# Kernel optimization log

Hardware: AMD Instinct MI355X
Metric: run time of the kernel (lower is better)

Reference implementation:

```python
import jax, jax.numpy as jnp
import numpy as np

# Static graph layout: B equal-sized graphs so per-graph k is constant (jit-friendly).
NUM_GRAPHS = 128
NODES_PER_GRAPH = 1024
NUM_NODES = NUM_GRAPHS * NODES_PER_GRAPH  # 131072
NUM_EDGES = NUM_NODES * 32               # 4194304
CHANNELS = 256
RATIO = 0.5
K = max(1, int(NODES_PER_GRAPH * RATIO))  # 512, matches max(1, int(count*ratio))


def setup_inputs() -> dict:
    key = jax.random.key(0)
    k0, k1, k2, k3 = jax.random.split(key, 4)
    x = jax.random.normal(k0, (NUM_NODES, CHANNELS), dtype=jnp.float32)
    edge_index = jax.random.randint(k1, (2, NUM_EDGES), 0, NUM_NODES, dtype=jnp.int64)
    batch = (jnp.arange(NUM_NODES, dtype=jnp.int64) // NODES_PER_GRAPH)
    # score MLP params: Linear(C, C) -> tanh -> Linear(C, 1)
    s = 1.0 / np.sqrt(CHANNELS)
    W1 = jax.random.uniform(k2, (CHANNELS, CHANNELS), jnp.float32, -s, s)
    b1 = jnp.zeros((CHANNELS,), jnp.float32)
    W2 = jax.random.uniform(k3, (CHANNELS, 1), jnp.float32, -s, s)
    b2 = jnp.zeros((1,), jnp.float32)
    return {"x": x, "edge_index": edge_index, "batch": batch,
            "W1": W1, "b1": b1, "W2": W2, "b2": b2}


def reference(x, edge_index, batch, W1, b1, W2, b2):
    # Note: SAGPool.forward computes a GNN score then discards it and calls
    # super().forward, which recomputes scores with the self.score MLP. The GNN
    # path is dead code (and would error in torch); the effective math is below.
    scores = (jnp.tanh(x @ W1 + b1) @ W2 + b2)[:, 0]  # [num_nodes]

    # Per-graph top-k, vectorized across all graphs (equal-sized segments).
    s = scores.reshape(NUM_GRAPHS, NODES_PER_GRAPH)
    top_s, top_i = jax.lax.top_k(s, K)  # descending per graph, matches torch.topk
    offsets = (jnp.arange(NUM_GRAPHS, dtype=top_i.dtype) * NODES_PER_GRAPH)[:, None]
    perm = (top_i + offsets).reshape(-1)  # [B*K] global indices, graphs in order

    x_pooled = x[perm]
    batch_pooled = batch[perm]
    scores_pooled = top_s.reshape(-1)

    # Edge filtering: keep edges whose both endpoints survive.
    keep = jnp.zeros((NUM_NODES,), dtype=bool).at[perm].set(True)
    row, col = edge_index
    edge_mask = keep[row] & keep[col]
    # Static-shape compaction: stable-sort kept edges to the front, pad with -1.
    order = jnp.argsort(~edge_mask, stable=True)
    edge_index_pooled = jnp.where(edge_mask[order][None, :], edge_index[:, order], -1)

    return x_pooled, edge_index_pooled, batch_pooled, perm, scores_pooled
```

## Files before the change

### kernel.cpp

```cpp
#include <hip/hip_runtime.h>
#include <hip/hip_bf16.h>

#define NG 128
#define NPG 1024
#define NN (NG * NPG)
#define NE (NN * 32)
#define CH 256
#define KSEL 512

#define CAP 128
#define EPS 0.02f

#define OUT_X      0
#define OUT_EDGE   16777216
#define OUT_BATCH  25165824
#define OUT_PERM   25231360
#define OUT_SCORES 25296896

#define WS_SCORES  0
#define WS_KEEP    524288
#define WS_COUNTS  540672
#define WS_OFFSETS 544768
#define WS_BFRAG   548864
#define WS_BIDX    679936
#define WS_BSCORE  745472
#define WS_BN      811008
#define WS_BLO     811520

typedef __attribute__((ext_vector_type(8))) short bf16x8;
typedef __attribute__((ext_vector_type(4))) float f32x4;

__device__ __forceinline__ unsigned short f2bf(float f) {
    unsigned int b = __float_as_uint(f);
    return (unsigned short)((b + 0x7fffu + ((b >> 16) & 1u)) >> 16);
}

__device__ __forceinline__ float tanh_fast(float h) {
    const float e = __expf(2.0f * h);
    return 1.0f - 2.0f / (e + 1.0f);
}

__global__ __launch_bounds__(256)
void k_cvtW(const float* __restrict__ W1, unsigned short* __restrict__ W1b,
            unsigned int* __restrict__ keep_bits)
{
    const int t = blockIdx.x * 256 + threadIdx.x;
    if (t < NN / 32) keep_bits[t] = 0u;
    const int s    = t >> 10;
    const int rem  = t & 1023;
    const int n    = rem >> 6;
    const int lane = rem & 63;
    const int kbase = s * 32 + (lane >> 4) * 8;
    const int col   = n * 16 + (lane & 15);
    unsigned short u[8];
    #pragma unroll
    for (int j = 0; j < 8; ++j)
        u[j] = f2bf(W1[(size_t)(kbase + j) * CH + col]);
    uint4 v;
    v.x = u[0] | ((unsigned int)u[1] << 16);
    v.y = u[2] | ((unsigned int)u[3] << 16);
    v.z = u[4] | ((unsigned int)u[5] << 16);
    v.w = u[6] | ((unsigned int)u[7] << 16);
    *(uint4*)&W1b[(size_t)t * 8] = v;
}

__global__ __launch_bounds__(256, 3)
void k_mfma_scores(const float* __restrict__ x, const unsigned short* __restrict__ W1b,
                   const float* __restrict__ b1, const float* __restrict__ W2,
                   const float* __restrict__ b2, float* __restrict__ scores)
{
    __shared__ __align__(16) short As[64 * 256];
    __shared__ float epi[4][64];

    const int tid = threadIdx.x;
    const int w_  = tid >> 6;
    const int l   = tid & 63;
    const int n0  = blockIdx.x * 64;

    #pragma unroll
    for (int it = 0; it < 16; ++it) {
        const int flat = it * 1024 + tid * 4;
        const int row = flat >> 8;
        const int c   = flat & 255;
        const float4 v = *(const float4*)&x[(size_t)(n0 + row) * CH + c];
        uint2 p;
        p.x = f2bf(v.x) | ((unsigned int)f2bf(v.y) << 16);
        p.y = f2bf(v.z) | ((unsigned int)f2bf(v.w) << 16);
        const int byte = (row * 512 + c * 2) ^ ((row & 7) << 4);
        *(uint2*)((char*)As + byte) = p;
    }
    __syncthreads();

    f32x4 acc[4][4];
    #pragma unroll
    for (int m = 0; m < 4; ++m)
        #pragma unroll
        for (int n = 0; n < 4; ++n)
            acc[m][n] = (f32x4){0.f, 0.f, 0.f, 0.f};

    const unsigned short* Wl = W1b + l * 8;
    bf16x8 bc[4], bn[4];
    #pragma unroll
    for (int ni = 0; ni < 4; ++ni)
        bc[ni] = *(const bf16x8*)&Wl[(size_t)(w_ * 4 + ni) * 512];

    #pragma unroll
    for (int s = 0; s < 8; ++s) {
        if (s < 7) {
            #pragma unroll
            for (int ni = 0; ni < 4; ++ni)
                bn[ni] = *(const bf16x8*)&Wl[(size_t)((s + 1) * 16 + w_ * 4 + ni) * 512];
        }
        bf16x8 a[4];
        #pragma unroll
        for (int m = 0; m < 4; ++m) {
            const int row  = m * 16 + (l & 15);
            const int byte = (row * 512 + s * 64 + ((l >> 4) * 16)) ^ ((l & 7) << 4);
            a[m] = *(const bf16x8*)((const char*)As + byte);
        }
        #pragma unroll
        for (int ni = 0; ni < 4; ++ni)
            #pragma unroll
            for (int m = 0; m < 4; ++m)
                acc[m][ni] = __builtin_amdgcn_mfma_f32_16x16x32_bf16(a[m], bc[ni], acc[m][ni], 0, 0, 0);
        #pragma unroll
        for (int ni = 0; ni < 4; ++ni) bc[ni] = bn[ni];
    }

    float part[16];
    #pragma unroll
    for (int i = 0; i < 16; ++i) part[i] = 0.f;
    #pragma unroll
    for (int ni = 0; ni < 4; ++ni) {
        const int col = w_ * 64 + ni * 16 + (l & 15);
        const float b1c = b1[col];
        const float w2c = W2[col];
        #pragma unroll
        for (int m = 0; m < 4; ++m)
            #pragma unroll
            for (int r = 0; r < 4; ++r)
                part[m * 4 + r] += tanh_fast(acc[m][ni][r] + b1c) * w2c;
    }
    #pragma unroll
    for (int off = 1; off < 16; off <<= 1)
        #pragma unroll
        for (int i = 0; i < 16; ++i)
            part[i] += __shfl_xor(part[i], off, 64);

    if ((l & 15) == 0) {
        const int gq = l >> 4;
        #pragma unroll
        for (int m = 0; m < 4; ++m)
            #pragma unroll
            for (int r = 0; r < 4; ++r)
                epi[w_][m * 16 + gq * 4 + r] = part[m * 4 + r];
    }
    __syncthreads();
    if (tid < 64)
        scores[n0 + tid] = epi[0][tid] + epi[1][tid] + epi[2][tid] + epi[3][tid] + b2[0];
}

__global__ __launch_bounds__(256)
void k_topk(const float* __restrict__ scores, float* __restrict__ out,
            unsigned int* __restrict__ keep_bits, int* __restrict__ band_idx,
            int* __restrict__ band_n, int* __restrict__ band_lo)
{
    __shared__ float    sf[1024];
    __shared__ unsigned uk[1024];
    __shared__ int      hist[256];
    __shared__ int      cge[256];
    __shared__ unsigned s_prefix;
    __shared__ int      s_rank;
    __shared__ int      wtot[4];

    const int g = blockIdx.x;
    const int t = threadIdx.x;

    #pragma unroll
    for (int h = 0; h < 4; ++h) {
        const int i = h * 256 + t;
        const float f = scores[g * NPG + i];
        sf[i] = f;
        const unsigned b = __float_as_uint(f);
        uk[i] = (b & 0x80000000u) ? ~b : (b | 0x80000000u);
    }
    if (t == 0) { s_prefix = 0u; s_rank = KSEL; }
    __syncthreads();

    const unsigned pmaskv[4] = {0u, 0xFF000000u, 0xFFFF0000u, 0xFFFFFF00u};
    #pragma unroll
    for (int pass = 0; pass < 4; ++pass) {
        const int shift = 24 - pass * 8;
        hist[t] = 0;
        __syncthreads();
        const unsigned pm  = pmaskv[pass];
        const unsigned pfx = s_prefix;
        #pragma unroll
        for (int h = 0; h < 4; ++h) {
            const unsigned u = uk[h * 256 + t];
            if ((u & pm) == pfx) atomicAdd(&hist[(u >> shift) & 255], 1);
        }
        __syncthreads();
        cge[t] = hist[t];
        __syncthreads();
        #pragma unroll
        for (int off = 1; off < 256; off <<= 1) {
            const int v = (t + off < 256) ? cge[t + off] : 0;
            __syncthreads();
            cge[t] += v;
            __syncthreads();
        }
        const int r = s_rank;
        const int above = (t == 255) ? 0 : cge[t + 1];
        if (cge[t] >= r && above < r) {
            s_prefix = pfx | ((unsigned)t << shift);
            s_rank   = r - above;
        }
        __syncthreads();
    }

    const unsigned u512 = s_prefix;
    const unsigned fb = (u512 & 0x80000000u) ? (u512 & 0x7FFFFFFFu) : ~u512;
    const float tau = __uint_as_float(fb);

    bool cert[4], bnd[4];
    int myc = 0, myb = 0;
    #pragma unroll
    for (int j = 0; j < 4; ++j) {
        const float f = sf[t * 4 + j];
        cert[j] = (f > tau + EPS);
        bnd[j]  = (!cert[j]) && (f >= tau - EPS);
        myc += cert[j] ? 1 : 0;
        myb += bnd[j] ? 1 : 0;
    }
    const int pack = (myc << 16) | myb;
    const int lane = t & 63, w = t >> 6;
    int incl = pack;
    #pragma unroll
    for (int off = 1; off < 64; off <<= 1) {
        const int v = __shfl_up(incl, off, 64);
        if (lane >= off) incl += v;
    }
    if (lane == 63) wtot[w] = incl;
    __syncthreads();
    int wbase = 0;
    for (int i = 0; i < w; ++i) wbase += wtot[i];
    const int excl = wbase + incl - pack;
    int cpos = excl >> 16;
    int bpos = excl & 0xFFFF;
    const int total = wtot[0] + wtot[1] + wtot[2] + wtot[3];

    #pragma unroll
    for (int j = 0; j < 4; ++j) {
        const int li = t * 4 + j;
        if (cert[j]) {
            const int gi = g * NPG + li;
            out[OUT_PERM   + g * KSEL + cpos] = (float)gi;
            out[OUT_SCORES + g * KSEL + cpos] = sf[li];
            atomicOr(&keep_bits[gi >> 5], 1u << (gi & 31));
            ++cpos;
        } else if (bnd[j]) {
            if (bpos < CAP) band_idx[g * CAP + bpos] = li;
            ++bpos;
        }
    }
    out[OUT_BATCH + g * KSEL + t]       = (float)g;
    out[OUT_BATCH + g * KSEL + t + 256] = (float)g;
    if (t == 0) {
        band_lo[g] = (total >> 16);
        band_n[g]  = min(total & 0xFFFF, CAP);
    }
}

__global__ __launch_bounds__(256, 2)
void k_rescore(const float* __restrict__ x, const float* __restrict__ W1,
               const float* __restrict__ b1, const float* __restrict__ W2,
               const float* __restrict__ b2, const int* __restrict__ band_idx,
               const int* __restrict__ band_n, float* __restrict__ band_scores)
{
    const int g = blockIdx.x >> 2;
    const int c0 = (blockIdx.x & 3) * 32;
    if (band_n[g] <= c0) return;

    __shared__ __align__(16) float W1s[16][CH];
    __shared__ __align__(16) float Xs[32][16];

    const int tid = threadIdx.x;
    const int w_  = tid >> 6;
    const int l   = tid & 63;

    int iv = 0;
    if (w_ < 2) iv = band_idx[g * CAP + c0 + w_ * 16 + (l >> 2)] & 1023;
    const float* xg = x + ((size_t)g * NPG + iv) * CH;

    const float4 b1v = *(const float4*)&b1[l * 4];
    float acc[8][4];
    #pragma unroll
    for (int n = 0; n < 8; ++n) {
        acc[n][0] = b1v.x; acc[n][1] = b1v.y; acc[n][2] = b1v.z; acc[n][3] = b1v.w;
    }

    for (int kc = 0; kc < 16; ++kc) {
        __syncthreads();
        #pragma unroll
        for (int it = 0; it < 4; ++it) {
            const float* gp = W1 + (size_t)kc * (16 * CH) + (w_ * 4 + it) * CH + l * 4;
            float* lb = &W1s[0][0] + (w_ * 4 + it) * CH;
            __builtin_amdgcn_global_load_lds(
                (const __attribute__((address_space(1))) void*)gp,
                (__attribute__((address_space(3))) void*)lb, 16, 0, 0);
        }
        if (w_ < 2) {
            const float* gp = xg + kc * 16 + (l & 3) * 4;
            float* lb = &Xs[0][0] + w_ * 256;
            __builtin_amdgcn_global_load_lds(
                (const __attribute__((address_space(1))) void*)gp,
                (__attribute__((address_space(3))) void*)lb, 16, 0, 0);
        }
        __syncthreads();

        #pragma unroll
        for (int kq = 0; kq < 4; ++kq) {
            const int k4 = kq * 4;
            const float4 wv0 = *(const float4*)&W1s[k4 + 0][l * 4];
            const float4 wv1 = *(const float4*)&W1s[k4 + 1][l * 4];
            const float4 wv2 = *(const float4*)&W1s[k4 + 2][l * 4];
            const float4 wv3 = *(const float4*)&W1s[k4 + 3][l * 4];
            #pragma unroll
            for (int n = 0; n < 8; ++n) {
                const float4 xv = *(const float4*)&Xs[w_ * 8 + n][k4];
                acc[n][0] = fmaf(xv.x, wv0.x, acc[n][0]);
                acc[n][1] = fmaf(xv.x, wv0.y, acc[n][1]);
                acc[n][2] = fmaf(xv.x, wv0.z, acc[n][2]);
                acc[n][3] = fmaf(xv.x, wv0.w, acc[n][3]);
                acc[n][0] = fmaf(xv.y, wv1.x, acc[n][0]);
                acc[n][1] = fmaf(xv.y, wv1.y, acc[n][1]);
                acc[n][2] = fmaf(xv.y, wv1.z, acc[n][2]);
                acc[n][3] = fmaf(xv.y, wv1.w, acc[n][3]);
                acc[n][0] = fmaf(xv.z, wv2.x, acc[n][0]);
                acc[n][1] = fmaf(xv.z, wv2.y, acc[n][1]);
                acc[n][2] = fmaf(xv.z, wv2.z, acc[n][2]);
                acc[n][3] = fmaf(xv.z, wv2.w, acc[n][3]);
                acc[n][0] = fmaf(xv.w, wv3.x, acc[n][0]);
                acc[n][1] = fmaf(xv.w, wv3.y, acc[n][1]);
                acc[n][2] = fmaf(xv.w, wv3.z, acc[n][2]);
                acc[n][3] = fmaf(xv.w, wv3.w, acc[n][3]);
            }
        }
    }

    const float4 w2v = *(const float4*)&W2[l * 4];
    const float  bb  = b2[0];
    float s_[8];
    #pragma unroll
    for (int n = 0; n < 8; ++n) {
        s_[n] = tanhf(acc[n][0]) * w2v.x + tanhf(acc[n][1]) * w2v.y
              + tanhf(acc[n][2]) * w2v.z + tanhf(acc[n][3]) * w2v.w;
    }
    #pragma unroll
    for (int off = 1; off < 64; off <<= 1)
        #pragma unroll
        for (int n = 0; n < 8; ++n)
            s_[n] += __shfl_xor(s_[n], off, 64);

    if (l == 0) {
        #pragma unroll
        for (int n = 0; n < 8; ++n)
            band_scores[g * CAP + c0 + w_ * 8 + n] = s_[n] + bb;
    }
}

__global__ __launch_bounds__(64)
void k_bandsel(const float* __restrict__ band_scores, const int* __restrict__ band_idx,
               const int* __restrict__ band_n, const int* __restrict__ band_lo,
               float* __restrict__ out, unsigned int* __restrict__ keep_bits)
{
    __shared__ float bs[CAP];
    __shared__ int   bi[CAP];
    const int g = blockIdx.x;
    const int t = threadIdx.x;
    const int n  = band_n[g];
    const int lo = band_lo[g];
    int needed = KSEL - lo;
    if (needed > n) needed = n;

    #pragma unroll
    for (int h = 0; h < 2; ++h) {
        const int q = t + h * 64;
        const bool valid = q < n;
        bs[q] = valid ? band_scores[g * CAP + q] : -3.402823466e+38f;
        bi[q] = valid ? band_idx[g * CAP + q] : (NPG + q);
    }
    __syncthreads();
    for (int size = 2; size <= CAP; size <<= 1) {
        for (int stride = size >> 1; stride > 0; stride >>= 1) {
            __syncthreads();
            const int lo_i = ((t & ~(stride - 1)) << 1) | (t & (stride - 1));
            const int hi_i = lo_i + stride;
            const bool dirDesc = ((lo_i & size) == 0);
            const float va = bs[lo_i], vb = bs[hi_i];
            const int ia = bi[lo_i], ib = bi[hi_i];
            const bool aB = (va > vb) || (va == vb && ia < ib);
            if (aB != dirDesc) {
                bs[lo_i] = vb; bs[hi_i] = va;
                bi[lo_i] = ib; bi[hi_i] = ia;
            }
        }
    }
    __syncthreads();
    #pragma unroll
    for (int h = 0; h < 2; ++h) {
        const int s = t + h * 64;
        if (s < needed) {
            const int li = bi[s];
            const int gi = g * NPG + li;
            out[OUT_PERM   + g * KSEL + lo + s] = (float)gi;
            out[OUT_SCORES + g * KSEL + lo + s] = bs[s];
            atomicOr(&keep_bits[gi >> 5], 1u << (gi & 31));
        }
    }
}

__global__ __launch_bounds__(256)
void k_gather(const float* __restrict__ x, const float* __restrict__ perm_f,
              float* __restrict__ out_x)
{
    const int row  = blockIdx.x * 4 + (threadIdx.x >> 6);
    const int lane = threadIdx.x & 63;
    const int pi = (int)perm_f[row];
    const float4* src = (const float4*)&x[(size_t)pi * CH];
    float4* dst = (float4*)&out_x[(size_t)row * CH];
    dst[lane] = src[lane];
}

__global__ __launch_bounds__(256)
void k_edgecount(const int* __restrict__ ei, const unsigned int* __restrict__ keep_bits,
                 int* __restrict__ counts, float* __restrict__ out_edge)
{
    const int t = threadIdx.x;
    const float4 neg = make_float4(-1.f, -1.f, -1.f, -1.f);
    #pragma unroll
    for (int q = 0; q < 4; ++q) {
        ((float4*)out_edge)[(size_t)blockIdx.x * 1024 + q * 256 + t] = neg;
        ((float4*)(out_edge + NE))[(size_t)blockIdx.x * 1024 + q * 256 + t] = neg;
    }

    const size_t base = (size_t)blockIdx.x * 4096 + (size_t)t * 16;
    const int* rowp = ei;
    const int* colp = ei + NE;
    int rv[16], cv[16];
    #pragma unroll
    for (int q = 0; q < 4; ++q) {
        int4 r4 = *(const int4*)&rowp[base + q * 4];
        int4 c4 = *(const int4*)&colp[base + q * 4];
        rv[q*4+0]=r4.x; rv[q*4+1]=r4.y; rv[q*4+2]=r4.z; rv[q*4+3]=r4.w;
        cv[q*4+0]=c4.x; cv[q*4+1]=c4.y; cv[q*4+2]=c4.z; cv[q*4+3]=c4.w;
    }
    int cnt = 0;
    #pragma unroll
    for (int q = 0; q < 16; ++q)
        cnt += (int)((keep_bits[rv[q] >> 5] >> (rv[q] & 31)) &
                     (keep_bits[cv[q] >> 5] >> (cv[q] & 31)) & 1u);

    #pragma unroll
    for (int off = 1; off < 64; off <<= 1) cnt += __shfl_xor(cnt, off, 64);
    __shared__ int wsum[4];
    if ((t & 63) == 0) wsum[t >> 6] = cnt;
    __syncthreads();
    if (t == 0) counts[blockIdx.x] = wsum[0] + wsum[1] + wsum[2] + wsum[3];
}

__global__ __launch_bounds__(1024)
void k_scan(const int* __restrict__ counts, int* __restrict__ offsets)
{
    __shared__ int tmp[1024];
    const int t = threadIdx.x;
    const int c = counts[t];
    tmp[t] = c;
    __syncthreads();
    for (int off = 1; off < 1024; off <<= 1) {
        int v = (t >= off) ? tmp[t - off] : 0;
        __syncthreads();
        tmp[t] += v;
        __syncthreads();
    }
    offsets[t] = tmp[t] - c;
}

__global__ __launch_bounds__(256)
void k_scatter(const int* __restrict__ ei, const unsigned int* __restrict__ keep_bits,
               const int* __restrict__ offsets, float* __restrict__ out_edge)
{
    const int t = threadIdx.x;
    const size_t base = (size_t)blockIdx.x * 4096 + (size_t)t * 16;
    const int* rowp = ei;
    const int* colp = ei + NE;
    int rv[16], cv[16];
    #pragma unroll
    for (int q = 0; q < 4; ++q) {
        int4 r4 = *(const int4*)&rowp[base + q * 4];
        int4 c4 = *(const int4*)&colp[base + q * 4];
        rv[q*4+0]=r4.x; rv[q*4+1]=r4.y; rv[q*4+2]=r4.z; rv[q*4+3]=r4.w;
        cv[q*4+0]=c4.x; cv[q*4+1]=c4.y; cv[q*4+2]=c4.z; cv[q*4+3]=c4.w;
    }
    unsigned m = 0; int cnt = 0;
    #pragma unroll
    for (int q = 0; q < 16; ++q) {
        const bool kk = ((keep_bits[rv[q] >> 5] >> (rv[q] & 31)) &
                         (keep_bits[cv[q] >> 5] >> (cv[q] & 31)) & 1u) != 0u;
        m |= ((unsigned)kk) << q;
        cnt += (int)kk;
    }
    const int lane = t & 63, w = t >> 6;
    int incl = cnt;
    #pragma unroll
    for (int off = 1; off < 64; off <<= 1) {
        int v = __shfl_up(incl, off, 64);
        if (lane >= off) incl += v;
    }
    __shared__ int wtot[4];
    if (lane == 63) wtot[w] = incl;
    __syncthreads();
    int wbase = 0;
    for (int i = 0; i < w; ++i) wbase += wtot[i];
    int pos = offsets[blockIdx.x] + wbase + (incl - cnt);
    #pragma unroll
    for (int q = 0; q < 16; ++q) {
        if (m & (1u << q)) {
            out_edge[pos]      = (float)rv[q];
            out_edge[NE + pos] = (float)cv[q];
            ++pos;
        }
    }
}

extern "C" void kernel_launch(void* const* d_in, const int* in_sizes, int n_in,
                              void* d_out, int out_size, void* d_ws, size_t ws_size,
                              hipStream_t stream)
{
    const float* x  = (const float*)d_in[0];
    const int*   ei = (const int*)d_in[1];
    const float* W1 = (const float*)d_in[3];
    const float* b1 = (const float*)d_in[4];
    const float* W2 = (const float*)d_in[5];
    const float* b2 = (const float*)d_in[6];

    float* out = (float*)d_out;
    char*  ws  = (char*)d_ws;
    float*          scores    = (float*)(ws + WS_SCORES);
    unsigned int*   keep_bits = (unsigned int*)(ws + WS_KEEP);
    int*            counts    = (int*)(ws + WS_COUNTS);
    int*            offsets   = (int*)(ws + WS_OFFSETS);
    unsigned short* W1b       = (unsigned short*)(ws + WS_BFRAG);
    int*            band_idx  = (int*)(ws + WS_BIDX);
    float*          band_sc   = (float*)(ws + WS_BSCORE);
    int*            band_n    = (int*)(ws + WS_BN);
    int*            band_lo   = (int*)(ws + WS_BLO);

    k_cvtW<<<32, 256, 0, stream>>>(W1, W1b, keep_bits);
    k_mfma_scores<<<NN / 64, 256, 0, stream>>>(x, W1b, b1, W2, b2, scores);
    k_topk<<<NG, 256, 0, stream>>>(scores, out, keep_bits, band_idx, band_n, band_lo);
    k_rescore<<<NG * (CAP / 32), 256, 0, stream>>>(x, W1, b1, W2, b2, band_idx, band_n, band_sc);
    k_bandsel<<<NG, 64, 0, stream>>>(band_sc, band_idx, band_n, band_lo, out, keep_bits);
    k_gather<<<(NG * KSEL) / 4, 256, 0, stream>>>(x, out + OUT_PERM, out + OUT_X);
    k_edgecount<<<NE / 4096, 256, 0, stream>>>(ei, keep_bits, counts, out + OUT_EDGE);
    k_scan<<<1, 1024, 0, stream>>>(counts, offsets);
    k_scatter<<<NE / 4096, 256, 0, stream>>>(ei, keep_bits, offsets, out + OUT_EDGE);
}
```

Measured before the change: 161.6 us.

## Rewrite band rescore as one wavefront per node with direct W1 reads

The fp32 rescore kernel for borderline top-k candidates drops its LDS-tiled 32-node block GEMM. Each wavefront now computes one band node's score, reading W1 straight from global memory (L2-resident) and looping over slots with stride 32. Grid-level parallelism doubles and blocks skip the sync-heavy staging, so sparse bands finish with less wasted work. The cost is that W1 is re-read per node and no longer shared across rows through LDS.

```diff
diff --git a/kernel.cpp b/kernel.cpp
--- a/kernel.cpp
+++ b/kernel.cpp
@@ -272,101 +272,50 @@
     }
 }
 
-__global__ __launch_bounds__(256, 2)
+__global__ __launch_bounds__(256)
 void k_rescore(const float* __restrict__ x, const float* __restrict__ W1,
                const float* __restrict__ b1, const float* __restrict__ W2,
                const float* __restrict__ b2, const int* __restrict__ band_idx,
                const int* __restrict__ band_n, float* __restrict__ band_scores)
 {
-    const int g = blockIdx.x >> 2;
-    const int c0 = (blockIdx.x & 3) * 32;
-    if (band_n[g] <= c0) return;
-
-    __shared__ __align__(16) float W1s[16][CH];
-    __shared__ __align__(16) float Xs[32][16];
-
-    const int tid = threadIdx.x;
-    const int w_  = tid >> 6;
-    const int l   = tid & 63;
-
-    int iv = 0;
-    if (w_ < 2) iv = band_idx[g * CAP + c0 + w_ * 16 + (l >> 2)] & 1023;
-    const float* xg = x + ((size_t)g * NPG + iv) * CH;
+    const int g  = blockIdx.x >> 3;
+    const int w_ = threadIdx.x >> 6;
+    const int l  = threadIdx.x & 63;
+    const int bn = band_n[g];
+    const int slot0 = (blockIdx.x & 7) * 4 + w_;
 
     const float4 b1v = *(const float4*)&b1[l * 4];
-    float acc[8][4];
-    #pragma unroll
-    for (int n = 0; n < 8; ++n) {
-        acc[n][0] = b1v.x; acc[n][1] = b1v.y; acc[n][2] = b1v.z; acc[n][3] = b1v.w;
-    }
-
-    for (int kc = 0; kc < 16; ++kc) {
-        __syncthreads();
-        #pragma unroll
-        for (int it = 0; it < 4; ++it) {
-            const float* gp = W1 + (size_t)kc * (16 * CH) + (w_ * 4 + it) * CH + l * 4;
-            float* lb = &W1s[0][0] + (w_ * 4 + it) * CH;
-            __builtin_amdgcn_global_load_lds(
-                (const __attribute__((address_space(1))) void*)gp,
-                (__attribute__((address_space(3))) void*)lb, 16, 0, 0);
-        }
-        if (w_ < 2) {
-            const float* gp = xg + kc * 16 + (l & 3) * 4;
-            float* lb = &Xs[0][0] + w_ * 256;
-            __builtin_amdgcn_global_load_lds(
-                (const __attribute__((address_space(1))) void*)gp,
-                (__attribute__((address_space(3))) void*)lb, 16, 0, 0);
-        }
-        __syncthreads();
-
-        #pragma unroll
-        for (int kq = 0; kq < 4; ++kq) {
-            const int k4 = kq * 4;
-            const float4 wv0 = *(const float4*)&W1s[k4 + 0][l * 4];
-            const float4 wv1 = *(const float4*)&W1s[k4 + 1][l * 4];
-            const float4 wv2 = *(const float4*)&W1s[k4 + 2][l * 4];
-            const float4 wv3 = *(const float4*)&W1s[k4 + 3][l * 4];
-            #pragma unroll
-            for (int n = 0; n < 8; ++n) {
-                const float4 xv = *(const float4*)&Xs[w_ * 8 + n][k4];
-                acc[n][0] = fmaf(xv.x, wv0.x, acc[n][0]);
-                acc[n][1] = fmaf(xv.x, wv0.y, acc[n][1]);
-                acc[n][2] = fmaf(xv.x, wv0.z, acc[n][2]);
-                acc[n][3] = fmaf(xv.x, wv0.w, acc[n][3]);
-                acc[n][0] = fmaf(xv.y, wv1.x, acc[n][0]);
-                acc[n][1] = fmaf(xv.y, wv1.y, acc[n][1]);
-                acc[n][2] = fmaf(xv.y, wv1.z, acc[n][2]);
-                acc[n][3] = fmaf(xv.y, wv1.w, acc[n][3]);
-                acc[n][0] = fmaf(xv.z, wv2.x, acc[n][0]);
-                acc[n][1] = fmaf(xv.z, wv2.y, acc[n][1]);
-                acc[n][2] = fmaf(xv.z, wv2.z, acc[n][2]);
-                acc[n][3] = fmaf(xv.z, wv2.w, acc[n][3]);
-                acc[n][0] = fmaf(xv.w, wv3.x, acc[n][0]);
-                acc[n][1] = fmaf(xv.w, wv3.y, acc[n][1]);
-                acc[n][2] = fmaf(xv.w, wv3.z, acc[n][2]);
-                acc[n][3] = fmaf(xv.w, wv3.w, acc[n][3]);
-            }
-        }
-    }
-
     const float4 w2v = *(const float4*)&W2[l * 4];
     const float  bb  = b2[0];
-    float s_[8];
-    #pragma unroll
-    for (int n = 0; n < 8; ++n) {
-        s_[n] = tanhf(acc[n][0]) * w2v.x + tanhf(acc[n][1]) * w2v.y
-              + tanhf(acc[n][2]) * w2v.z + tanhf(acc[n][3]) * w2v.w;
-    }
-    #pragma unroll
-    for (int off = 1; off < 64; off <<= 1)
-        #pragma unroll
-        for (int n = 0; n < 8; ++n)
-            s_[n] += __shfl_xor(s_[n], off, 64);
-
-    if (l == 0) {
-        #pragma unroll
-        for (int n = 0; n < 8; ++n)
-            band_scores[g * CAP + c0 + w_ * 8 + n] = s_[n] + bb;
+
+    for (int slot = slot0; slot < bn; slot += 32) {
+        const int node = band_idx[g * CAP + slot] & 1023;
+        const float* xr = x + ((size_t)g * NPG + node) * CH;
+
+        float a0 = b1v.x, a1 = b1v.y, a2 = b1v.z, a3 = b1v.w;
+        #pragma unroll 8
+        for (int kc = 0; kc < 64; ++kc) {
+            const float4 xs  = *(const float4*)(xr + kc * 4);
+            const float4 w0  = *(const float4*)&W1[(size_t)(kc * 4 + 0) * CH + l * 4];
+            const float4 w1r = *(const float4*)&W1[(size_t)(kc * 4 + 1) * CH + l * 4];
+            const float4 w2r = *(const float4*)&W1[(size_t)(kc * 4 + 2) * CH + l * 4];
+            const float4 w3r = *(const float4*)&W1[(size_t)(kc * 4 + 3) * CH + l * 4];
+            a0 = fmaf(xs.x, w0.x, a0);  a1 = fmaf(xs.x, w0.y, a1);
+            a2 = fmaf(xs.x, w0.z, a2);  a3 = fmaf(xs.x, w0.w, a3);
+            a0 = fmaf(xs.y, w1r.x, a0); a1 = fmaf(xs.y, w1r.y, a1);
+            a2 = fmaf(xs.y, w1r.z, a2); a3 = fmaf(xs.y, w1r.w, a3);
+            a0 = fmaf(xs.z, w2r.x, a0); a1 = fmaf(xs.z, w2r.y, a1);
+            a2 = fmaf(xs.z, w2r.z, a2); a3 = fmaf(xs.z, w2r.w, a3);
+            a0 = fmaf(xs.w, w3r.x, a0); a1 = fmaf(xs.w, w3r.y, a1);
+            a2 = fmaf(xs.w, w3r.z, a2); a3 = fmaf(xs.w, w3r.w, a3);
+        }
+        float part = tanhf(a0) * w2v.x + tanhf(a1) * w2v.y
+                   + tanhf(a2) * w2v.z + tanhf(a3) * w2v.w;
+        #pragma unroll
+        for (int off = 1; off < 64; off <<= 1)
+            part += __shfl_xor(part, off, 64);
+        if (l == 0)
+            band_scores[g * CAP + slot] = part + bb;
     }
 }
 
@@ -560,7 +509,7 @@
     k_cvtW<<<32, 256, 0, stream>>>(W1, W1b, keep_bits);
     k_mfma_scores<<<NN / 64, 256, 0, stream>>>(x, W1b, b1, W2, b2, scores);
     k_topk<<<NG, 256, 0, stream>>>(scores, out, keep_bits, band_idx, band_n, band_lo);
-    k_rescore<<<NG * (CAP / 32), 256, 0, stream>>>(x, W1, b1, W2, b2, band_idx, band_n, band_sc);
+    k_rescore<<<NG * 8, 256, 0, stream>>>(x, W1, b1, W2, b2, band_idx, band_n, band_sc);
     k_bandsel<<<NG, 64, 0, stream>>>(band_sc, band_idx, band_n, band_lo, out, keep_bits);
     k_gather<<<(NG * KSEL) / 4, 256, 0, stream>>>(x, out + OUT_PERM, out + OUT_X);
     k_edgecount<<<NE / 4096, 256, 0, stream>>>(ei, keep_bits, counts, out + OUT_EDGE);
```

Result: slower. 235.1 us (+45.5%).
